# Optimization experiments

Hardware: AMD Instinct MI355X
Metric: run time of the kernel (lower is better)

Reference implementation:

```python
import jax, jax.numpy as jnp
import numpy as np

NB = 64        # number of chains = batch.max()+1 (static for reshape)
NPER = 131072  # points per chain
NTYPES = 16
NITER = 10
ACC = 1e-9


def setup_inputs() -> dict:
    key = jax.random.key(0)
    k1, k2, k3 = jax.random.split(key, 3)
    x = jax.random.normal(k1, (NB * NPER, 3), dtype=jnp.float32)
    d0 = jax.random.uniform(k2, (NTYPES, NTYPES), dtype=jnp.float32, minval=0.5, maxval=1.5)
    z = jax.random.randint(k3, (NB * NPER,), 0, NTYPES)
    batch = jnp.repeat(jnp.arange(NB), NPER)  # contiguous chain ids
    return {"x": x, "d0": d0, "batch": batch, "z": z}


def _diffT(C):
    # adjoint of the forward difference stencil: [nb, n-1, 3] -> [nb, n, 3]
    mid = C[:, :-1] - C[:, 1:]
    return jnp.concatenate([-C[:, :1], mid, C[:, -1:]], axis=1)


def _constraint(r, d):
    # r: [nb, n, 3], d: [nb, n-1, 1]; c_i = |r_{i+1}-r_i|^2 - d_i^2
    dx = r[:, 1:] - r[:, :-1]
    c = jnp.sum(dx * dx, axis=-1, keepdims=True) - d * d
    return c, dx


def _line_search(x_sg, lam_sg, d_sg, alpha0, cnorm):
    # emulates the torch.no_grad() backtracking line search
    def eval_ctry(a):
        rt = (x_sg - a * lam_sg).reshape(NB, NPER, 3)
        ct, _ = _constraint(rt, d_sg)
        return jnp.sum(ct * ct)

    def cond(s):
        return ~s[3]

    def body(s):
        alpha, lsiter, _, _ = s
        ctry = eval_ctry(alpha)
        ok = ctry < cnorm
        new_alpha = jnp.where(ok, alpha, alpha * 0.5)
        new_lsiter = jnp.where(ok, lsiter, lsiter + 1)
        done = ok | (new_lsiter > 10)
        return (new_alpha, new_lsiter, ctry, done)

    init = (alpha0, jnp.int32(0), jnp.float32(jnp.inf), jnp.bool_(False))
    alpha, lsiter, ctry, _ = jax.lax.while_loop(cond, body, init)
    # if no backtracking happened and not converged, grow the step
    alpha = jnp.where((lsiter == 0) & (ctry > ACC), alpha * 1.5, alpha)
    return alpha, ctry


def _forward(x, d0, z):
    z2 = z.reshape(NB, NPER)
    # gather-based distance lookup for consecutive pairs: [NB, NPER-1, 1]
    d = d0[z2[:, :-1], z2[:, 1:]].astype(x.dtype)[..., None]
    d_sg = jax.lax.stop_gradient(d)
    x_cur = x
    alpha = jnp.float32(0.0)
    done = jnp.bool_(False)
    for j in range(NITER):
        r = x_cur.reshape(NB, NPER, 3)
        c, dx = _constraint(r, d)               # [NB, NPER-1, 1], [NB, NPER-1, 3]
        lam = 2.0 * _diffT(c * dx)              # dConstraintT2: [NB, NPER, 3]
        lam_x = lam.reshape(-1, 3)
        cnorm = jnp.sum(c * c)
        x_sg = jax.lax.stop_gradient(x_cur)
        lam_sg = jax.lax.stop_gradient(lam_x)
        cnorm_sg = jax.lax.stop_gradient(cnorm)
        alpha0 = (1.0 / jnp.linalg.norm(lam_sg)) if j == 0 else alpha
        alpha_j, ctry = _line_search(x_sg, lam_sg, d_sg, alpha0, cnorm_sg)
        x_new = x_cur - alpha_j * lam_x
        # freeze updates after convergence (emulates the torch early break)
        x_cur = jnp.where(done, x_cur, x_new)
        alpha = jnp.where(done, alpha, alpha_j)
        done = done | (ctry < ACC)
    return x_cur


def reference(x, d0, batch, z):
    # batch only encodes nb = batch.max()+1; layout is contiguous chains (static NB)
    return _forward(x, d0, z)
```

## Files before the change

kernel.cpp:

```cpp
#include <hip/hip_runtime.h>

#define NB 64
#define NPER 131072
#define NTYPES 16
#define NITER 10
#define ACCV 1e-9

#define TB 256
#define TILES_PER_CHAIN (NPER / TB)
#define TILES_TOTAL (NB * TILES_PER_CHAIN)
#define FBLOCKS 2048
#define TPB (TILES_TOTAL / FBLOCKS)

struct PCState {
  double alpha;
  double alpha_step;
  int done;
  int do_update;
  unsigned ticket;
};

__device__ inline double wave_sum64(double v) {
  #pragma unroll
  for (int o = 32; o > 0; o >>= 1) v += __shfl_down(v, o, 64);
  return v;
}

__global__ void pc_init(PCState* st) {
  st->alpha = 0.0;
  st->alpha_step = 0.0;
  st->done = 0;
  st->do_update = 1;
  st->ticket = 0u;
}

template <int MODE>
__global__ __launch_bounds__(TB) void pc_fused(
    const float* __restrict__ xin, float* __restrict__ xout,
    const int* __restrict__ z, const float* __restrict__ d0,
    PCState* st, double* __restrict__ part, int iter) {
  __shared__ float xs[(TB + 5) * 3];
  __shared__ float xn[(TB + 3) * 3];
  __shared__ float Cold[(TB + 4) * 3];
  __shared__ float ds2[TB + 4];
  __shared__ float Cnew[(TB + 2) * 3];
  __shared__ float cnw[TB + 2];
  __shared__ float dxn[(TB + 2) * 3];
  __shared__ int zs[TB + 5];
  __shared__ float d0s[NTYPES * NTYPES];
  __shared__ double redl[5][TB / 64];
  __shared__ int islast;

  const int tid = threadIdx.x;
  d0s[tid] = d0[tid];
  const float alpha = (MODE == 0 || !st->do_update) ? 0.f : (float)st->alpha_step;
  double s0 = 0, s1 = 0, s2 = 0, s3 = 0, s4 = 0;

  for (int tt = 0; tt < TPB; ++tt) {
    const int tile = blockIdx.x * TPB + tt;
    const int b = tile / TILES_PER_CHAIN;
    const int t = tile % TILES_PER_CHAIN;
    const int P0 = t * TB;
    const int base = b * NPER;
    __syncthreads();

    {
      const int gf0 = (base + P0 - 2) * 3;
      const int lo = base * 3, hi = (base + NPER) * 3;
      for (int f = tid; f < (TB + 5) * 3; f += TB) {
        const int g = gf0 + f;
        xs[f] = (g >= lo && g < hi) ? xin[g] : 0.f;
      }
      for (int q = tid; q < TB + 5; q += TB) {
        const int p = P0 - 2 + q;
        zs[q] = (p >= 0 && p < NPER) ? z[base + p] : 0;
      }
    }
    __syncthreads();

    for (int q = tid; q < TB + 4; q += TB) {
      const int j = P0 - 2 + q;
      float cx = 0.f, cy = 0.f, cz = 0.f, dd2 = 0.f;
      if (j >= 0 && j <= NPER - 2) {
        const int l = q * 3;
        const float ax = xs[l + 3] - xs[l + 0];
        const float ay = xs[l + 4] - xs[l + 1];
        const float az = xs[l + 5] - xs[l + 2];
        const float dd = d0s[zs[q] * NTYPES + zs[q + 1]];
        dd2 = dd * dd;
        const float c = ax * ax + ay * ay + az * az - dd2;
        cx = c * ax; cy = c * ay; cz = c * az;
      }
      Cold[q * 3 + 0] = cx; Cold[q * 3 + 1] = cy; Cold[q * 3 + 2] = cz;
      ds2[q] = dd2;
    }
    __syncthreads();

    for (int q = tid; q < TB + 3; q += TB) {
      const int p = P0 - 1 + q;
      float nx = 0.f, ny = 0.f, nz = 0.f;
      if (p >= 0 && p < NPER) {
        const int l = (q + 1) * 3;
        const int cb = q * 3;
        const float lx = 2.f * (Cold[cb + 0] - Cold[cb + 3]);
        const float ly = 2.f * (Cold[cb + 1] - Cold[cb + 4]);
        const float lz = 2.f * (Cold[cb + 2] - Cold[cb + 5]);
        nx = xs[l + 0] - alpha * lx;
        ny = xs[l + 1] - alpha * ly;
        nz = xs[l + 2] - alpha * lz;
        if (MODE != 0 && p >= P0 && p < P0 + TB) {
          const int g = (base + p) * 3;
          xout[g + 0] = nx; xout[g + 1] = ny; xout[g + 2] = nz;
        }
      }
      xn[q * 3 + 0] = nx; xn[q * 3 + 1] = ny; xn[q * 3 + 2] = nz;
    }

    if (MODE != 2) {
      __syncthreads();
      for (int q = tid; q < TB + 2; q += TB) {
        const int j = P0 - 1 + q;
        float c = 0.f, ax = 0.f, ay = 0.f, az = 0.f;
        if (j >= 0 && j <= NPER - 2) {
          const int l = q * 3;
          ax = xn[l + 3] - xn[l + 0];
          ay = xn[l + 4] - xn[l + 1];
          az = xn[l + 5] - xn[l + 2];
          c = ax * ax + ay * ay + az * az - ds2[q + 1];
        }
        cnw[q] = c;
        dxn[q * 3 + 0] = ax; dxn[q * 3 + 1] = ay; dxn[q * 3 + 2] = az;
        Cnew[q * 3 + 0] = c * ax; Cnew[q * 3 + 1] = c * ay; Cnew[q * 3 + 2] = c * az;
      }
      __syncthreads();

      const int i = P0 + tid;
      if (i <= NPER - 2) {
        const int l = (tid + 1) * 3;
        const float gx = 2.f * (2.f * Cnew[l + 0] - Cnew[l - 3] - Cnew[l + 3]);
        const float gy = 2.f * (2.f * Cnew[l + 1] - Cnew[l - 2] - Cnew[l + 4]);
        const float gz = 2.f * (2.f * Cnew[l + 2] - Cnew[l - 1] - Cnew[l + 5]);
        const float A = gx * gx + gy * gy + gz * gz;
        const float Bv = -2.f * (dxn[l + 0] * gx + dxn[l + 1] * gy + dxn[l + 2] * gz);
        const float c = cnw[tid + 1];
        s0 += (double)c * (double)c;
        s1 += 2.0 * (double)c * (double)Bv;
        s2 += (double)Bv * (double)Bv + 2.0 * (double)c * (double)A;
        s3 += 2.0 * (double)A * (double)Bv;
        s4 += (double)A * (double)A;
      }
    }
  }

  if (MODE == 2) return;

  {
    double v[5] = {s0, s1, s2, s3, s4};
    const int wave = tid >> 6, lane = tid & 63;
    #pragma unroll
    for (int k = 0; k < 5; ++k) {
      const double w = wave_sum64(v[k]);
      if (lane == 0) redl[k][wave] = w;
    }
    __syncthreads();
    if (tid == 0) {
      #pragma unroll
      for (int k = 0; k < 5; ++k)
        part[k * FBLOCKS + blockIdx.x] =
            redl[k][0] + redl[k][1] + redl[k][2] + redl[k][3];
      __threadfence();
      const unsigned tk = atomicAdd(&st->ticket, 1u);
      islast = (tk == FBLOCKS - 1) ? 1 : 0;
    }
    __syncthreads();
    if (!islast) return;
  }

  __threadfence();
  {
    double v[5] = {0, 0, 0, 0, 0};
    for (int i = tid; i < FBLOCKS; i += TB) {
      #pragma unroll
      for (int k = 0; k < 5; ++k) v[k] += part[k * FBLOCKS + i];
    }
    const int wave = tid >> 6, lane = tid & 63;
    #pragma unroll
    for (int k = 0; k < 5; ++k) {
      const double w = wave_sum64(v[k]);
      if (lane == 0) redl[k][wave] = w;
    }
    __syncthreads();
    if (tid == 0) {
      double S[5];
      #pragma unroll
      for (int k = 0; k < 5; ++k)
        S[k] = redl[k][0] + redl[k][1] + redl[k][2] + redl[k][3];
      const double cnorm = S[0];
      double alpha2 = (iter == 0) ? 1.0 / sqrt(-0.5 * S[1]) : st->alpha;
      int lsiter = 0;
      double ctry;
      for (;;) {
        ctry = S[0] + alpha2 * (S[1] + alpha2 * (S[2] + alpha2 * (S[3] + alpha2 * S[4])));
        if (ctry < cnorm) break;
        alpha2 *= 0.5;
        if (++lsiter > 10) break;
      }
      if (lsiter == 0 && ctry > ACCV) alpha2 *= 1.5;
      const int done_prev = st->done;
      st->alpha_step = alpha2;
      st->do_update = done_prev ? 0 : 1;
      if (!done_prev) st->alpha = alpha2;
      st->done = done_prev | ((ctry < ACCV) ? 1 : 0);
      st->ticket = 0u;
    }
  }
}

extern "C" void kernel_launch(void* const* d_in, const int* in_sizes, int n_in,
                              void* d_out, int out_size, void* d_ws, size_t ws_size,
                              hipStream_t stream) {
  const float* d0 = (const float*)d_in[1];
  const int* z = (const int*)d_in[3];
  float* ping = (float*)d_in[0];
  float* dout = (float*)d_out;
  PCState* st = (PCState*)d_ws;
  double* part = (double*)((char*)d_ws + 256);
  const size_t xbytes = (size_t)NB * NPER * 3 * sizeof(float);

  hipMemcpyAsync(dout, ping, xbytes, hipMemcpyDeviceToDevice, stream);
  pc_init<<<1, 1, 0, stream>>>(st);
  pc_fused<0><<<FBLOCKS, TB, 0, stream>>>(dout, dout, z, d0, st, part, 0);
  float* a = dout;
  float* bufb = ping;
  for (int j = 1; j <= 9; ++j) {
    pc_fused<1><<<FBLOCKS, TB, 0, stream>>>(a, bufb, z, d0, st, part, j);
    float* tmp = a; a = bufb; bufb = tmp;
  }
  pc_fused<2><<<FBLOCKS, TB, 0, stream>>>(a, bufb, z, d0, st, part, 10);
}
```

Before: 1.527 ms.

## Enlarge tiles, vectorize loads with register prefetch, and recompute stencils to drop shared buffers

Each tile now covers 1024 points instead of 256, so halo overhead and barriers per point go down. The x and z tiles are loaded as float4/int4 into registers for the next tile while the current one is being computed, overlapping global memory latency with compute. Intermediate shared arrays (Cold, Cnew, dxn, cnw) are replaced by recomputing the neighbouring constraint terms in registers, which leaves fewer syncs per tile. Per-tile partial sums are now accumulated in float before being promoted to double, which loses some precision. The launch bound also asks for 4 blocks per SM.

Measured after the change: 1.329 ms. -13.0%, faster.

```diff
diff --git a/kernel.cpp b/kernel.cpp
--- a/kernel.cpp
+++ b/kernel.cpp
@@ -3,14 +3,19 @@
 #define NB 64
 #define NPER 131072
 #define NTYPES 16
-#define NITER 10
 #define ACCV 1e-9
 
 #define TB 256
-#define TILES_PER_CHAIN (NPER / TB)
+#define TILE_PTS 1024
+#define TILES_PER_CHAIN (NPER / TILE_PTS)
 #define TILES_TOTAL (NB * TILES_PER_CHAIN)
 #define FBLOCKS 2048
 #define TPB (TILES_TOTAL / FBLOCKS)
+#define NTOT (NB * NPER)
+#define FX_MAX (NTOT * 3 / 4)
+#define ZX_MAX (NTOT / 4)
+#define XS_F4 774
+#define ZS_I4 258
 
 struct PCState {
   double alpha;
@@ -35,120 +40,129 @@
 }
 
 template <int MODE>
-__global__ __launch_bounds__(TB) void pc_fused(
+__global__ __launch_bounds__(TB, 4) void pc_fused(
     const float* __restrict__ xin, float* __restrict__ xout,
-    const int* __restrict__ z, const float* __restrict__ d0,
+    const int* __restrict__ zin, const float* __restrict__ d0,
     PCState* st, double* __restrict__ part, int iter) {
-  __shared__ float xs[(TB + 5) * 3];
-  __shared__ float xn[(TB + 3) * 3];
-  __shared__ float Cold[(TB + 4) * 3];
-  __shared__ float ds2[TB + 4];
-  __shared__ float Cnew[(TB + 2) * 3];
-  __shared__ float cnw[TB + 2];
-  __shared__ float dxn[(TB + 2) * 3];
-  __shared__ int zs[TB + 5];
+  __shared__ float4 xs4[XS_F4];
+  __shared__ int4 zs4[ZS_I4];
+  __shared__ float xn[(TILE_PTS + 3) * 3];
+  __shared__ float ds2[TILE_PTS + 4];
   __shared__ float d0s[NTYPES * NTYPES];
   __shared__ double redl[5][TB / 64];
   __shared__ int islast;
+  const float* xs = (const float*)xs4;
+  const int* zs = (const int*)zs4;
 
   const int tid = threadIdx.x;
   d0s[tid] = d0[tid];
   const float alpha = (MODE == 0 || !st->do_update) ? 0.f : (float)st->alpha_step;
+  const float4* x4 = (const float4*)xin;
+  const int4* z4 = (const int4*)zin;
+
   double s0 = 0, s1 = 0, s2 = 0, s3 = 0, s4 = 0;
-
+  float4 pf0, pf1, pf2, pf3 = make_float4(0.f, 0.f, 0.f, 0.f);
+  int4 pz0, pz1 = make_int4(0, 0, 0, 0);
+
+  auto pf_issue = [&](int tile) {
+    const int b_ = tile / TILES_PER_CHAIN;
+    const int p0_ = b_ * NPER + (tile % TILES_PER_CHAIN) * TILE_PTS - 4;
+    const int fx0 = (p0_ * 3) >> 2;
+    const int zx0 = p0_ >> 2;
+    pf0 = x4[min(max(fx0 + tid, 0), FX_MAX - 1)];
+    pf1 = x4[min(max(fx0 + 256 + tid, 0), FX_MAX - 1)];
+    pf2 = x4[min(max(fx0 + 512 + tid, 0), FX_MAX - 1)];
+    if (tid < XS_F4 - 768) pf3 = x4[min(max(fx0 + 768 + tid, 0), FX_MAX - 1)];
+    pz0 = z4[min(max(zx0 + tid, 0), ZX_MAX - 1)];
+    if (tid < ZS_I4 - 256) pz1 = z4[min(max(zx0 + 256 + tid, 0), ZX_MAX - 1)];
+  };
+
+  pf_issue(blockIdx.x * TPB);
   for (int tt = 0; tt < TPB; ++tt) {
     const int tile = blockIdx.x * TPB + tt;
-    const int b = tile / TILES_PER_CHAIN;
-    const int t = tile % TILES_PER_CHAIN;
-    const int P0 = t * TB;
-    const int base = b * NPER;
-    __syncthreads();
-
-    {
-      const int gf0 = (base + P0 - 2) * 3;
-      const int lo = base * 3, hi = (base + NPER) * 3;
-      for (int f = tid; f < (TB + 5) * 3; f += TB) {
-        const int g = gf0 + f;
-        xs[f] = (g >= lo && g < hi) ? xin[g] : 0.f;
-      }
-      for (int q = tid; q < TB + 5; q += TB) {
-        const int p = P0 - 2 + q;
-        zs[q] = (p >= 0 && p < NPER) ? z[base + p] : 0;
-      }
-    }
-    __syncthreads();
-
-    for (int q = tid; q < TB + 4; q += TB) {
-      const int j = P0 - 2 + q;
-      float cx = 0.f, cy = 0.f, cz = 0.f, dd2 = 0.f;
-      if (j >= 0 && j <= NPER - 2) {
-        const int l = q * 3;
-        const float ax = xs[l + 3] - xs[l + 0];
-        const float ay = xs[l + 4] - xs[l + 1];
-        const float az = xs[l + 5] - xs[l + 2];
-        const float dd = d0s[zs[q] * NTYPES + zs[q + 1]];
-        dd2 = dd * dd;
-        const float c = ax * ax + ay * ay + az * az - dd2;
-        cx = c * ax; cy = c * ay; cz = c * az;
-      }
-      Cold[q * 3 + 0] = cx; Cold[q * 3 + 1] = cy; Cold[q * 3 + 2] = cz;
-      ds2[q] = dd2;
-    }
-    __syncthreads();
-
-    for (int q = tid; q < TB + 3; q += TB) {
+    const int P0 = (tile % TILES_PER_CHAIN) * TILE_PTS;
+    const int base = (tile / TILES_PER_CHAIN) * NPER;
+
+    xs4[tid] = pf0; xs4[tid + 256] = pf1; xs4[tid + 512] = pf2;
+    if (tid < XS_F4 - 768) xs4[tid + 768] = pf3;
+    zs4[tid] = pz0;
+    if (tid < ZS_I4 - 256) zs4[tid + 256] = pz1;
+    __syncthreads();
+
+    if (tt + 1 < TPB) pf_issue(tile + 1);
+    for (int q = tid; q < TILE_PTS + 3; q += TB) {
       const int p = P0 - 1 + q;
-      float nx = 0.f, ny = 0.f, nz = 0.f;
-      if (p >= 0 && p < NPER) {
-        const int l = (q + 1) * 3;
-        const int cb = q * 3;
-        const float lx = 2.f * (Cold[cb + 0] - Cold[cb + 3]);
-        const float ly = 2.f * (Cold[cb + 1] - Cold[cb + 4]);
-        const float lz = 2.f * (Cold[cb + 2] - Cold[cb + 5]);
-        nx = xs[l + 0] - alpha * lx;
-        ny = xs[l + 1] - alpha * ly;
-        nz = xs[l + 2] - alpha * lz;
-        if (MODE != 0 && p >= P0 && p < P0 + TB) {
-          const int g = (base + p) * 3;
-          xout[g + 0] = nx; xout[g + 1] = ny; xout[g + 2] = nz;
+      float Ca[2][3]; float dd2v[2];
+      #pragma unroll
+      for (int k = 0; k < 2; ++k) {
+        const int j = p - 1 + k;
+        const int xi = (q + 2 + k) * 3;
+        if (j >= 0 && j <= NPER - 2) {
+          const float ax = xs[xi + 3] - xs[xi + 0];
+          const float ay = xs[xi + 4] - xs[xi + 1];
+          const float az = xs[xi + 5] - xs[xi + 2];
+          const float dd = d0s[zs[q + 2 + k] * NTYPES + zs[q + 3 + k]];
+          dd2v[k] = dd * dd;
+          const float c = ax * ax + ay * ay + az * az - dd2v[k];
+          Ca[k][0] = c * ax; Ca[k][1] = c * ay; Ca[k][2] = c * az;
+        } else {
+          dd2v[k] = 0.f; Ca[k][0] = 0.f; Ca[k][1] = 0.f; Ca[k][2] = 0.f;
         }
       }
-      xn[q * 3 + 0] = nx; xn[q * 3 + 1] = ny; xn[q * 3 + 2] = nz;
-    }
+      if (MODE != 2) { ds2[q] = dd2v[0]; ds2[q + 1] = dd2v[1]; }
+      const int xi = (q + 3) * 3;
+      const float nx = xs[xi + 0] - alpha * 2.f * (Ca[0][0] - Ca[1][0]);
+      const float ny = xs[xi + 1] - alpha * 2.f * (Ca[0][1] - Ca[1][1]);
+      const float nz = xs[xi + 2] - alpha * 2.f * (Ca[0][2] - Ca[1][2]);
+      if (MODE != 2) {
+        const bool pv = (p >= 0) && (p < NPER);
+        const int o = q * 3;
+        xn[o + 0] = pv ? nx : 0.f;
+        xn[o + 1] = pv ? ny : 0.f;
+        xn[o + 2] = pv ? nz : 0.f;
+      }
+      if (MODE != 0 && p >= P0 && p < P0 + TILE_PTS) {
+        const int g = (base + p) * 3;
+        xout[g + 0] = nx; xout[g + 1] = ny; xout[g + 2] = nz;
+      }
+    }
+    __syncthreads();
 
     if (MODE != 2) {
-      __syncthreads();
-      for (int q = tid; q < TB + 2; q += TB) {
-        const int j = P0 - 1 + q;
-        float c = 0.f, ax = 0.f, ay = 0.f, az = 0.f;
-        if (j >= 0 && j <= NPER - 2) {
-          const int l = q * 3;
-          ax = xn[l + 3] - xn[l + 0];
-          ay = xn[l + 4] - xn[l + 1];
-          az = xn[l + 5] - xn[l + 2];
-          c = ax * ax + ay * ay + az * az - ds2[q + 1];
+      float q0 = 0, q1 = 0, q2 = 0, q3 = 0, q4 = 0;
+      for (int qq = tid; qq < TILE_PTS; qq += TB) {
+        const int i = P0 + qq;
+        if (i <= NPER - 2) {
+          float CN[3][3]; float cI = 0.f, dxv[3] = {0.f, 0.f, 0.f};
+          #pragma unroll
+          for (int k = 0; k < 3; ++k) {
+            const int j = i - 1 + k;
+            if (j >= 0 && j <= NPER - 2) {
+              const int o = (qq + k) * 3;
+              const float ax = xn[o + 3] - xn[o + 0];
+              const float ay = xn[o + 4] - xn[o + 1];
+              const float az = xn[o + 5] - xn[o + 2];
+              const float c = ax * ax + ay * ay + az * az - ds2[qq + k + 1];
+              CN[k][0] = c * ax; CN[k][1] = c * ay; CN[k][2] = c * az;
+              if (k == 1) { cI = c; dxv[0] = ax; dxv[1] = ay; dxv[2] = az; }
+            } else {
+              CN[k][0] = 0.f; CN[k][1] = 0.f; CN[k][2] = 0.f;
+            }
+          }
+          const float gx = 2.f * (2.f * CN[1][0] - CN[0][0] - CN[2][0]);
+          const float gy = 2.f * (2.f * CN[1][1] - CN[0][1] - CN[2][1]);
+          const float gz = 2.f * (2.f * CN[1][2] - CN[0][2] - CN[2][2]);
+          const float A = gx * gx + gy * gy + gz * gz;
+          const float Bv = -2.f * (dxv[0] * gx + dxv[1] * gy + dxv[2] * gz);
+          q0 += cI * cI;
+          q1 += 2.f * cI * Bv;
+          q2 += Bv * Bv + 2.f * cI * A;
+          q3 += 2.f * A * Bv;
+          q4 += A * A;
         }
-        cnw[q] = c;
-        dxn[q * 3 + 0] = ax; dxn[q * 3 + 1] = ay; dxn[q * 3 + 2] = az;
-        Cnew[q * 3 + 0] = c * ax; Cnew[q * 3 + 1] = c * ay; Cnew[q * 3 + 2] = c * az;
-      }
-      __syncthreads();
-
-      const int i = P0 + tid;
-      if (i <= NPER - 2) {
-        const int l = (tid + 1) * 3;
-        const float gx = 2.f * (2.f * Cnew[l + 0] - Cnew[l - 3] - Cnew[l + 3]);
-        const float gy = 2.f * (2.f * Cnew[l + 1] - Cnew[l - 2] - Cnew[l + 4]);
-        const float gz = 2.f * (2.f * Cnew[l + 2] - Cnew[l - 1] - Cnew[l + 5]);
-        const float A = gx * gx + gy * gy + gz * gz;
-        const float Bv = -2.f * (dxn[l + 0] * gx + dxn[l + 1] * gy + dxn[l + 2] * gz);
-        const float c = cnw[tid + 1];
-        s0 += (double)c * (double)c;
-        s1 += 2.0 * (double)c * (double)Bv;
-        s2 += (double)Bv * (double)Bv + 2.0 * (double)c * (double)A;
-        s3 += 2.0 * (double)A * (double)Bv;
-        s4 += (double)A * (double)A;
-      }
+      }
+      s0 += (double)q0; s1 += (double)q1; s2 += (double)q2;
+      s3 += (double)q3; s4 += (double)q4;
     }
   }
 
```
